# Kernel tuning notes

Hardware: AMD Instinct MI355X
Metric: run time of the kernel (lower is better)

Reference implementation:

```python
import jax, jax.numpy as jnp
import numpy as np
from jax import lax

HEADS, HEAD_DIM, DIM, DIM_OUT, EPS = 12, 64, 768, 768, 1e-5
REL_DIM = 2 * 56 - 1  # 2*max(q_size, kv_size) - 1


def setup_inputs():
    key = jax.random.key(0)
    ks = jax.random.split(key, 10)
    B, T, H, W = 4, 1, 56, 56
    N = 1 + T * H * W
    s = 0.02
    return {
        "x": jax.random.normal(ks[0], (B, N, DIM), jnp.float32),
        "Wqkv": jax.random.normal(ks[1], (DIM, 3 * DIM_OUT), jnp.float32) * s,
        "pool_q_w": jax.random.normal(ks[2], (HEAD_DIM, 1, 3, 3), jnp.float32) * 0.1,
        "pool_k_w": jax.random.normal(ks[3], (HEAD_DIM, 1, 3, 3), jnp.float32) * 0.1,
        "pool_v_w": jax.random.normal(ks[4], (HEAD_DIM, 1, 3, 3), jnp.float32) * 0.1,
        "gq": jnp.ones((HEAD_DIM,), jnp.float32), "bq": jnp.zeros((HEAD_DIM,), jnp.float32),
        "gk": jnp.ones((HEAD_DIM,), jnp.float32), "bk": jnp.zeros((HEAD_DIM,), jnp.float32),
        "gv": jnp.ones((HEAD_DIM,), jnp.float32), "bv": jnp.zeros((HEAD_DIM,), jnp.float32),
        "rel_pos_h": jax.random.normal(ks[5], (REL_DIM, HEAD_DIM), jnp.float32) * s,
        "rel_pos_w": jax.random.normal(ks[6], (REL_DIM, HEAD_DIM), jnp.float32) * s,
        "Wproj": jax.random.normal(ks[7], (DIM_OUT, DIM_OUT), jnp.float32) * s,
        "bproj": jnp.zeros((DIM_OUT,), jnp.float32),
        "T": 1, "H": 56, "W": 56,
    }


def _layernorm(y, g, b):
    mu = y.mean(-1, keepdims=True)
    var = ((y - mu) ** 2).mean(-1, keepdims=True)
    return (y - mu) * lax.rsqrt(var + EPS) * g + b


def _pool(t, w, stride, g, b, B, H, W):
    # t: (B, heads, 1 + H*W, head_dim). Split cls, depthwise conv over spatial body.
    cls, body = t[:, :, :1], t[:, :, 1:]
    y = body.reshape(B * HEADS, H, W, HEAD_DIM).transpose(0, 3, 1, 2)  # (BH, C, H, W)
    y = lax.conv_general_dilated(y, w, (stride, stride), [(1, 1), (1, 1)],
                                 feature_group_count=HEAD_DIM,
                                 dimension_numbers=("NCHW", "OIHW", "NCHW"))
    Ho, Wo = y.shape[2], y.shape[3]
    y = y.reshape(B, HEADS, HEAD_DIM, Ho * Wo).transpose(0, 1, 3, 2)
    y = jnp.concatenate([cls, y], axis=2)
    return _layernorm(y, g, b), Ho, Wo


def _forward(x, Wqkv, pool_q_w, pool_k_w, pool_v_w, gq, bq, gk, bk, gv, bv,
             rel_pos_h, rel_pos_w, Wproj, bproj, T, H, W):
    B, N, _ = x.shape
    scale = HEAD_DIM ** -0.5
    qkv = (x @ Wqkv).reshape(B, N, 3, HEADS, HEAD_DIM).transpose(2, 0, 3, 1, 4)
    q, k, v = qkv[0], qkv[1], qkv[2]  # (B, heads, N, head_dim)
    q, q_h, q_w = _pool(q, pool_q_w, 1, gq, bq, B, H, W)
    k, k_h, k_w = _pool(k, pool_k_w, 2, gk, bk, B, H, W)
    v, _, _ = _pool(v, pool_v_w, 2, gv, bv, B, H, W)
    attn = jnp.einsum("bhqd,bhkd->bhqk", q * scale, k)
    # relative position bias; index tables are static (shapes known at trace time)
    dh = (np.arange(q_h)[:, None] * max(k_h / q_h, 1.0)
          - np.arange(k_h)[None, :] * max(q_h / k_h, 1.0)
          + (k_h - 1) * max(q_h / k_h, 1.0)).astype(np.int32)
    dw = (np.arange(q_w)[:, None] * max(k_w / q_w, 1.0)
          - np.arange(k_w)[None, :] * max(q_w / k_w, 1.0)
          + (k_w - 1) * max(q_w / k_w, 1.0)).astype(np.int32)
    Rh, Rw = rel_pos_h[dh], rel_pos_w[dw]  # (q_h, k_h, c), (q_w, k_w, c)
    r_q = q[:, :, 1:].reshape(B, HEADS, q_h, q_w, HEAD_DIM)
    rel_h = jnp.einsum("byhwc,hkc->byhwk", r_q, Rh)
    rel_w = jnp.einsum("byhwc,wkc->byhwk", r_q, Rw)
    body = (attn[:, :, 1:, 1:].reshape(B, HEADS, q_h, q_w, k_h, k_w)
            + rel_h[..., None] + rel_w[..., None, :])
    attn = attn.at[:, :, 1:, 1:].set(body.reshape(B, HEADS, q_h * q_w, k_h * k_w))
    attn = jax.nn.softmax(attn, axis=-1)
    out = attn @ v
    out = out.at[:, :, 1:, :].add(q[:, :, 1:, :])  # residual pooling (skips cls)
    out = out.transpose(0, 2, 1, 3).reshape(B, -1, DIM_OUT)
    return out @ Wproj + bproj


def reference(x, Wqkv, pool_q_w, pool_k_w, pool_v_w, gq, bq, gk, bk, gv, bv,
              rel_pos_h, rel_pos_w, Wproj, bproj, T, H, W):
    return _forward(x, Wqkv, pool_q_w, pool_k_w, pool_v_w, gq, bq, gk, bk, gv, bv,
                    rel_pos_h, rel_pos_w, Wproj, bproj, T, H, W)
```

## Files before the change

kernel.cpp:

```cpp
#include <hip/hip_runtime.h>
#include <hip/hip_bf16.h>

#define BATCH 4
#define NTOK 3137
#define DIM 768
#define NHEAD 12
#define HD 64
#define QH 56
#define QW 56
#define NKEY 785
#define NKEYPAD 800
#define THREE_DIM 2304
#define MROWS (BATCH*NTOK)
#define QTILE 64
#define NQT 50
#define NBH 48
#define RELROWS (NBH*56)
#define XD 128

#define QSCALE 0.1803368801111204f
#define QUNSCALE 5.5451774444795625f
#define PADSUP  -43.3f

typedef __attribute__((ext_vector_type(8))) short bf16x8;
typedef __attribute__((ext_vector_type(4))) float f32x4;

__device__ __forceinline__ unsigned short f2bf(float f) {
    union { float f; unsigned u; } v; v.f = f;
    unsigned r = v.u + 0x7FFFu + ((v.u >> 16) & 1u);
    return (unsigned short)(r >> 16);
}
__device__ __forceinline__ float bf2f(unsigned short s) {
    union { unsigned u; float f; } v; v.u = (unsigned)s << 16; return v.f;
}
__device__ __forceinline__ int swz64(int x) { return x ^ (((x >> 6) & 7) << 4); }

__device__ __forceinline__ void gl16(const void* g, void* l) {
    __builtin_amdgcn_global_load_lds(
        (const __attribute__((address_space(1))) unsigned int*)g,
        (__attribute__((address_space(3))) unsigned int*)l, 16, 0, 0);
}

__global__ __launch_bounds__(256) void cvt_bf16(
    const float* __restrict__ in, unsigned short* __restrict__ outp, int n4)
{
    for (int i = blockIdx.x * 256 + threadIdx.x; i < n4; i += gridDim.x * 256) {
        float4 v = reinterpret_cast<const float4*>(in)[i];
        union { unsigned short s[4]; uint2 u; } o;
        o.s[0] = f2bf(v.x); o.s[1] = f2bf(v.y);
        o.s[2] = f2bf(v.z); o.s[3] = f2bf(v.w);
        reinterpret_cast<uint2*>(outp)[i] = o.u;
    }
}

__global__ __launch_bounds__(256) void cvt_rel(
    const float* __restrict__ h, const float* __restrict__ w,
    unsigned short* __restrict__ hb, unsigned short* __restrict__ wb)
{
    int i = blockIdx.x * 256 + threadIdx.x;
    const float* src; unsigned short* dst; int j;
    if (i < 1776)      { src = h; dst = hb; j = i; }
    else if (i < 3552) { src = w; dst = wb; j = i - 1776; }
    else return;
    float4 v = reinterpret_cast<const float4*>(src)[j];
    union { unsigned short s[4]; uint2 u; } o;
    o.s[0] = f2bf(v.x); o.s[1] = f2bf(v.y);
    o.s[2] = f2bf(v.z); o.s[3] = f2bf(v.w);
    reinterpret_cast<uint2*>(dst)[j] = o.u;
}

__global__ __launch_bounds__(256) void transpose_bf16_2(
    const float* __restrict__ W0, unsigned short* __restrict__ Wt0,
    const float* __restrict__ W1, unsigned short* __restrict__ Wt1)
{
    const float* W; unsigned short* Wt; int N;
    if (blockIdx.z == 0) { W = W0; Wt = Wt0; N = THREE_DIM; }
    else {
        if (blockIdx.x >= DIM / 32) return;
        W = W1; Wt = Wt1; N = DIM;
    }
    const int K = DIM;
    __shared__ float tile[32][33];
    int k0 = blockIdx.y * 32, n0 = blockIdx.x * 32;
    int t = threadIdx.x;
    int r = t >> 5, c = t & 31;
    #pragma unroll
    for (int p = 0; p < 4; ++p)
        tile[r + p * 8][c] = W[(size_t)(k0 + r + p * 8) * N + n0 + c];
    __syncthreads();
    #pragma unroll
    for (int p = 0; p < 4; ++p)
        Wt[(size_t)(n0 + r + p * 8) * K + k0 + c] = f2bf(tile[c][r + p * 8]);
}

__global__ __launch_bounds__(256, 3) void gemm_mfma(
    const unsigned short* __restrict__ A, const unsigned short* __restrict__ Bt,
    const float* __restrict__ bias, void* __restrict__ C,
    int M, int N, int K, int out_bf16)
{
    __shared__ __align__(16) char lds[49152];
    int t = threadIdx.x;
    int wave = t >> 6, lane = t & 63;
    int lm = lane & 15, lkg = lane >> 4;
    int wr = wave >> 1, wc = wave & 1;

    int gx = gridDim.x;
    int nwg = gx * gridDim.y;
    int lin = blockIdx.y * gx + blockIdx.x;
    int qq = nwg >> 3, rr = nwg & 7;
    int xcd = lin & 7, idx = lin >> 3;
    int newlin = (xcd < rr ? xcd * (qq + 1) : rr * (qq + 1) + (xcd - rr) * qq) + idx;
    int m0 = (newlin / gx) * 128, n0 = (newlin % gx) * 128;

    const unsigned short *gpa0, *gpa1, *gpb0, *gpb1;
    int la0, la1, lb0, lb1;
    {
        int o0 = t * 16, o1 = 4096 + t * 16;
        int r0 = o0 >> 6, s0 = ((o0 >> 4) & 3) ^ ((r0 >> 1) & 3);
        int r1 = o1 >> 6, s1 = ((o1 >> 4) & 3) ^ ((r1 >> 1) & 3);
        int ar0 = m0 + r0; if (ar0 >= M) ar0 = M - 1;
        int ar1 = m0 + r1; if (ar1 >= M) ar1 = M - 1;
        gpa0 = A + (size_t)ar0 * K + s0 * 8;  la0 = o0;
        gpa1 = A + (size_t)ar1 * K + s1 * 8;  la1 = o1;
        gpb0 = Bt + (size_t)(n0 + r0) * K + s0 * 8;  lb0 = 8192 + o0;
        gpb1 = Bt + (size_t)(n0 + r1) * K + s1 * 8;  lb1 = 8192 + o1;
    }

    f32x4 acc[4][4] = {};
    const int nt = K >> 5;

    gl16(gpa0, &lds[la0]); gl16(gpa1, &lds[la1]);
    gl16(gpb0, &lds[lb0]); gl16(gpb1, &lds[lb1]);
    gpa0 += 32; gpa1 += 32; gpb0 += 32; gpb1 += 32;
    gl16(gpa0, &lds[16384 + la0]); gl16(gpa1, &lds[16384 + la1]);
    gl16(gpb0, &lds[16384 + lb0]); gl16(gpb1, &lds[16384 + lb1]);
    gpa0 += 32; gpa1 += 32; gpb0 += 32; gpb1 += 32;

    int cur = 0;
    for (int tt = 0; tt < nt; ++tt) {
        if (tt + 1 < nt) asm volatile("s_waitcnt vmcnt(4)" ::: "memory");
        else             asm volatile("s_waitcnt vmcnt(0)" ::: "memory");
        __builtin_amdgcn_s_barrier();

        if (tt + 2 < nt) {
            int nx = cur + 2; if (nx >= 3) nx -= 3;
            char* nb = &lds[nx << 14];
            gl16(gpa0, nb + la0); gl16(gpa1, nb + la1);
            gl16(gpb0, nb + lb0); gl16(gpb1, nb + lb1);
            gpa0 += 32; gpa1 += 32; gpb0 += 32; gpb1 += 32;
        }

        char* base = &lds[cur << 14];
        bf16x8 af[4], bfr[4];
        #pragma unroll
        for (int m = 0; m < 4; ++m) {
            int row = wr * 64 + m * 16 + lm;
            af[m] = *reinterpret_cast<const bf16x8*>(
                base + row * 64 + ((lkg ^ ((row >> 1) & 3)) << 4));
        }
        #pragma unroll
        for (int n = 0; n < 4; ++n) {
            int row = wc * 64 + n * 16 + lm;
            bfr[n] = *reinterpret_cast<const bf16x8*>(
                base + 8192 + row * 64 + ((lkg ^ ((row >> 1) & 3)) << 4));
        }
        #pragma unroll
        for (int m = 0; m < 4; ++m)
            #pragma unroll
            for (int n = 0; n < 4; ++n)
                acc[m][n] = __builtin_amdgcn_mfma_f32_16x16x32_bf16(
                    af[m], bfr[n], acc[m][n], 0, 0, 0);

        cur = (cur == 2) ? 0 : cur + 1;
    }

    float bv[4];
    #pragma unroll
    for (int n = 0; n < 4; ++n)
        bv[n] = bias ? bias[n0 + wc * 64 + n * 16 + lm] : 0.f;
    #pragma unroll
    for (int m = 0; m < 4; ++m) {
        #pragma unroll
        for (int r = 0; r < 4; ++r) {
            int row = m0 + wr * 64 + m * 16 + lkg * 4 + r;
            if (row >= M) continue;
            #pragma unroll
            for (int n = 0; n < 4; ++n) {
                int col = n0 + wc * 64 + n * 16 + lm;
                float o = acc[m][n][r] + bv[n];
                if (out_bf16)
                    ((unsigned short*)C)[(size_t)row * N + col] = f2bf(o);
                else
                    ((float*)C)[(size_t)row * N + col] = o;
            }
        }
    }
}

__global__ __launch_bounds__(256) void pool_ln_rows(
    const unsigned short* __restrict__ qkvb, const float* __restrict__ w,
    const float* __restrict__ g, const float* __restrict__ beta,
    unsigned short* __restrict__ outp, int qi, int stride, int OH, int OW,
    int mode)
{
    __shared__ unsigned short ibuf[3 * 56 * 64];
    int bid = blockIdx.x;
    int orow = bid % OH;
    int bh = bid / OH;
    int head = bh % NHEAD, b = bh / NHEAD;
    int t = threadIdx.x;
    int wave = t >> 6, lane = t & 63;

    const unsigned short* src =
        qkvb + (size_t)b * NTOK * THREE_DIM + (size_t)qi * DIM + (size_t)head * HD;

    for (int i = t; i < 3 * 56 * 32; i += 256) {
        int pair = i >> 5, off = i & 31;
        int r = pair / 56, iw = pair % 56;
        int ih = orow * stride + r - 1;
        unsigned v = 0;
        if (ih >= 0 && ih < QH)
            v = *reinterpret_cast<const unsigned*>(
                src + (size_t)(1 + ih * QW + iw) * THREE_DIM + off * 2);
        *reinterpret_cast<unsigned*>(&ibuf[pair * 64 + off * 2]) = v;
    }

    float wreg[9];
    #pragma unroll
    for (int k = 0; k < 9; ++k) wreg[k] = w[lane * 9 + k];
    float gl = g[lane], bl = beta[lane];
    __syncthreads();

    int ntask = OW + ((orow == 0) ? 1 : 0);
    for (int task = wave; task < ntask; task += 4) {
        float val;
        int pos;
        if (task == OW) {
            val = bf2f(src[lane]);
            pos = 0;
        } else {
            int ow = task;
            float acc = 0.f;
            #pragma unroll
            for (int r = 0; r < 3; ++r) {
                #pragma unroll
                for (int c = 0; c < 3; ++c) {
                    int iwc = ow * stride + c - 1;
                    if (iwc < 0 || iwc >= QW) continue;
                    acc += bf2f(ibuf[(r * 56 + iwc) * 64 + lane]) * wreg[r * 3 + c];
                }
            }
            val = acc;
            pos = 1 + orow * OW + ow;
        }

        float mu = val;
        #pragma unroll
        for (int off = 32; off > 0; off >>= 1) mu += __shfl_xor(mu, off, 64);
        mu *= (1.f / 64.f);
        float dv = val - mu;
        float var = dv * dv;
        #pragma unroll
        for (int off = 32; off > 0; off >>= 1) var += __shfl_xor(var, off, 64);
        var *= (1.f / 64.f);
        float o = dv * rsqrtf(var + 1e-5f) * gl + bl;

        if (mode == 3) {
            unsigned short* row = outp + ((size_t)bh * NTOK + pos) * XD;
            row[lane] = f2bf(o * QSCALE);
            row[64 + lane] = (lane == 56) ? f2bf(PADSUP) : 0;
        } else if (mode == 1) {
            unsigned short* row = outp + ((size_t)bh * NKEYPAD + pos) * XD;
            row[lane] = f2bf(o);
            unsigned short ext = 0;
            if (pos > 0) {
                int kh = (pos - 1) / 28, kw = (pos - 1) % 28;
                if ((lane < 28 && lane == kh) ||
                    (lane >= 28 && lane < 56 && lane - 28 == kw))
                    ext = 0x3F80;
            }
            row[64 + lane] = ext;
        } else {
            outp[((size_t)bh * HD + lane) * NKEYPAD + pos] = f2bf(o);
        }
    }
}

__global__ __launch_bounds__(64) void pad_kv(
    unsigned short* __restrict__ kpx, unsigned short* __restrict__ vt16)
{
    int bh = blockIdx.x;
    int t = threadIdx.x;
    for (int pos = NKEY; pos < NKEYPAD; ++pos) {
        unsigned short* row = kpx + ((size_t)bh * NKEYPAD + pos) * XD;
        row[t] = 0;
        row[64 + t] = (t == 56) ? 0x3F80 : 0;
        vt16[((size_t)bh * HD + t) * NKEYPAD + pos] = 0;
    }
}

__global__ __launch_bounds__(256) void rel_mfma(
    const unsigned short* __restrict__ qpx, const unsigned short* __restrict__ rh,
    const unsigned short* __restrict__ rw, unsigned short* __restrict__ qpx_out)
{
    __shared__ char bbuf[4096];
    int X = blockIdx.x;
    int m0 = blockIdx.y * 256;
    int mode = blockIdx.z;
    const unsigned short* rtab = mode ? rw : rh;
    int t = threadIdx.x;
    int wave = t >> 6, lane = t & 63;
    int lm = lane & 15, lkg = lane >> 4;

    {
        int row = t >> 3, c8 = t & 7;
        int4 val = {0, 0, 0, 0};
        if (row < 28) {
            int dh = X - 2 * row + 54;
            val = *reinterpret_cast<const int4*>(rtab + (size_t)dh * HD + c8 * 8);
        }
        *reinterpret_cast<int4*>(&bbuf[row * 128 + ((c8 * 16) ^ ((row & 7) << 4))]) = val;
    }
    __syncthreads();

    int rbase = m0 + wave * 64 + lm;
    f32x4 acc[4][2] = {};
    #pragma unroll
    for (int kc = 0; kc < 2; ++kc) {
        bf16x8 bfrag[2];
        #pragma unroll
        for (int nb = 0; nb < 2; ++nb) {
            int row = nb * 16 + lm;
            bfrag[nb] = *reinterpret_cast<const bf16x8*>(
                &bbuf[row * 128 + (((kc * 4 + lkg) * 16) ^ ((row & 7) << 4))]);
        }
        #pragma unroll
        for (int m = 0; m < 4; ++m) {
            int rho = rbase + m * 16; if (rho > RELROWS - 1) rho = RELROWS - 1;
            int bh = rho / 56, rem = rho % 56;
            int pos1 = (mode == 0) ? X * 56 + rem : rem * 56 + X;
            const unsigned short* qsrc =
                qpx + ((size_t)bh * NTOK + 1 + pos1) * XD + kc * 32 + lkg * 8;
            bf16x8 af = *reinterpret_cast<const bf16x8*>(qsrc);
            acc[m][0] = __builtin_amdgcn_mfma_f32_16x16x32_bf16(af, bfrag[0], acc[m][0], 0, 0, 0);
            acc[m][1] = __builtin_amdgcn_mfma_f32_16x16x32_bf16(af, bfrag[1], acc[m][1], 0, 0, 0);
        }
    }

    #pragma unroll
    for (int m = 0; m < 4; ++m) {
        #pragma unroll
        for (int r = 0; r < 4; ++r) {
            int rho = m0 + wave * 64 + m * 16 + lkg * 4 + r;
            if (rho >= RELROWS) continue;
            int bh = rho / 56, rem = rho % 56;
            int pos1 = (mode == 0) ? X * 56 + rem : rem * 56 + X;
            unsigned short* dst =
                qpx_out + ((size_t)bh * NTOK + 1 + pos1) * XD + 64 + mode * 28;
            dst[lm] = f2bf(acc[m][0][r] * 8.f);
            if (lm < 12) dst[16 + lm] = f2bf(acc[m][1][r] * 8.f);
        }
    }
}

__global__ __launch_bounds__(256) void attn_mfma(
    const unsigned short* __restrict__ qpx, const unsigned short* __restrict__ kpx,
    const unsigned short* __restrict__ vt, unsigned short* __restrict__ outp)
{
    __shared__ __align__(16) char kbuf[3][8192];
    __shared__ __align__(16) char vbuf[3][4096];
    __shared__ __align__(16) char pbuf[4][1024];

    int bid0 = blockIdx.x;
    int bid = (bid0 & 7) * ((NBH * NQT) / 8) + (bid0 >> 3);
    int tile = bid % NQT;
    int bh = bid / NQT;
    int head = bh % NHEAD, b = bh / NHEAD;
    int q0 = tile * QTILE;
    int t = threadIdx.x;
    int wave = t >> 6, lane = t & 63;
    int lm = lane & 15, lkg = lane >> 4;

    const unsigned short* kb  = kpx + (size_t)bh * NKEYPAD * XD;
    const unsigned short* vtb = vt + (size_t)bh * HD * NKEYPAD;

    bf16x8 qf[4] = {};
    int qrow = q0 + wave * 16 + lm;
    if (qrow < NTOK) {
        const unsigned short* qs = qpx + ((size_t)bh * NTOK + qrow) * XD + lkg * 8;
        qf[0] = *reinterpret_cast<const bf16x8*>(qs);
        qf[1] = *reinterpret_cast<const bf16x8*>(qs + 32);
        qf[2] = *reinterpret_cast<const bf16x8*>(qs + 64);
        qf[3] = *reinterpret_cast<const bf16x8*>(qs + 96);
    }

    f32x4 oacc[4] = {};
    float osum[4] = {0.f, 0.f, 0.f, 0.f};

    int kr0 = t >> 4;
    int ks0 = (t & 15) ^ (kr0 & 7);
    int kr1 = kr0 + 16;
    const unsigned short* kp0 = kb + (size_t)kr0 * XD + ks0 * 8;
    const unsigned short* kp1 = kb + (size_t)kr1 * XD + ks0 * 8;
    int vr = t >> 2;
    int vs = (t & 3) ^ ((vr >> 1) & 3);
    const unsigned short* vp0 = vtb + (size_t)vr * NKEYPAD + vs * 8;
    int kd0 = wave * 1024, kd1 = 4096 + wave * 1024, vd = wave * 1024;

    const int NT = NKEYPAD / 32;

    gl16(kp0, &kbuf[0][kd0]); gl16(kp1, &kbuf[0][kd1]); gl16(vp0, &vbuf[0][vd]);
    kp0 += 32 * XD; kp1 += 32 * XD; vp0 += 32;
    gl16(kp0, &kbuf[1][kd0]); gl16(kp1, &kbuf[1][kd1]); gl16(vp0, &vbuf[1][vd]);
    kp0 += 32 * XD; kp1 += 32 * XD; vp0 += 32;

    int cur = 0;
    for (int jt = 0; jt < NT; ++jt) {
        if (jt + 1 < NT) asm volatile("s_waitcnt vmcnt(3)" ::: "memory");
        else             asm volatile("s_waitcnt vmcnt(0)" ::: "memory");
        __builtin_amdgcn_s_barrier();

        f32x4 acc0 = {0.f, 0.f, 0.f, 0.f}, acc1 = {0.f, 0.f, 0.f, 0.f};
        #pragma unroll
        for (int kc = 0; kc < 4; ++kc) {
            int sl = (kc * 4 + lkg) ^ (lm & 7);
            bf16x8 kf0 = *reinterpret_cast<const bf16x8*>(&kbuf[cur][lm * 256 + sl * 16]);
            acc0 = __builtin_amdgcn_mfma_f32_16x16x32_bf16(qf[kc], kf0, acc0, 0, 0, 0);
            bf16x8 kf1 = *reinterpret_cast<const bf16x8*>(&kbuf[cur][(16 + lm) * 256 + sl * 16]);
            acc1 = __builtin_amdgcn_mfma_f32_16x16x32_bf16(qf[kc], kf1, acc1, 0, 0, 0);
        }

        if (jt + 2 < NT) {
            int nx = cur + 2; if (nx >= 3) nx -= 3;
            gl16(kp0, &kbuf[nx][kd0]);
            gl16(kp1, &kbuf[nx][kd1]);
            gl16(vp0, &vbuf[nx][vd]);
            kp0 += 32 * XD; kp1 += 32 * XD; vp0 += 32;
        }

        #pragma unroll
        for (int nb = 0; nb < 2; ++nb) {
            f32x4 a = nb ? acc1 : acc0;
            #pragma unroll
            for (int r = 0; r < 4; ++r) {
                float e;
                asm("v_exp_f32 %0, %1" : "=v"(e) : "v"(a[r]));
                osum[r] += e;
                union { float f; unsigned u; } ue; ue.f = e;
                int baddr = (lkg * 4 + r) * 64 + (nb * 16 + lm) * 2;
                *reinterpret_cast<unsigned short*>(&pbuf[wave][swz64(baddr)]) =
                    (unsigned short)(ue.u >> 16);
            }
        }

        bf16x8 pf = *reinterpret_cast<const bf16x8*>(&pbuf[wave][swz64(lm * 64 + lkg * 16)]);
        #pragma unroll
        for (int db = 0; db < 4; ++db) {
            int row = db * 16 + lm;
            bf16x8 vf = *reinterpret_cast<const bf16x8*>(
                &vbuf[cur][row * 64 + ((lkg ^ ((row >> 1) & 3)) << 4)]);
            oacc[db] = __builtin_amdgcn_mfma_f32_16x16x32_bf16(pf, vf, oacc[db], 0, 0, 0);
        }

        cur = (cur == 2) ? 0 : cur + 1;
    }

    #pragma unroll
    for (int r = 0; r < 4; ++r) {
        float s = osum[r];
        s += __shfl_xor(s, 1, 64);
        s += __shfl_xor(s, 2, 64);
        s += __shfl_xor(s, 4, 64);
        s += __shfl_xor(s, 8, 64);
        osum[r] = 1.f / s;
    }
    #pragma unroll
    for (int r = 0; r < 4; ++r) {
        int qpos = q0 + wave * 16 + lkg * 4 + r;
        if (qpos >= NTOK) continue;
        unsigned short* orow = outp + ((size_t)b * NTOK + qpos) * DIM + (size_t)head * HD;
        const unsigned short* qres = qpx + ((size_t)bh * NTOK + qpos) * XD;
        #pragma unroll
        for (int db = 0; db < 4; ++db) {
            int d = db * 16 + lm;
            float o = oacc[db][r] * osum[r];
            if (qpos > 0) o += bf2f(qres[d]) * QUNSCALE;
            orow[d] = f2bf(o);
        }
    }
}

extern "C" void kernel_launch(void* const* d_in, const int* in_sizes, int n_in,
                              void* d_out, int out_size, void* d_ws, size_t ws_size,
                              hipStream_t stream) {
    const float* x     = (const float*)d_in[0];
    const float* Wqkv  = (const float*)d_in[1];
    const float* pqw   = (const float*)d_in[2];
    const float* pkw   = (const float*)d_in[3];
    const float* pvw   = (const float*)d_in[4];
    const float* gq    = (const float*)d_in[5];
    const float* bq    = (const float*)d_in[6];
    const float* gk    = (const float*)d_in[7];
    const float* bk    = (const float*)d_in[8];
    const float* gv    = (const float*)d_in[9];
    const float* bv    = (const float*)d_in[10];
    const float* rph   = (const float*)d_in[11];
    const float* rpw   = (const float*)d_in[12];
    const float* Wproj = (const float*)d_in[13];
    const float* bproj = (const float*)d_in[14];

    unsigned short* qkvb  = (unsigned short*)d_ws;
    unsigned short* qpx   = qkvb + (size_t)MROWS * THREE_DIM;
    unsigned short* kpx   = qpx + (size_t)NBH * NTOK * XD;
    unsigned short* vt16  = kpx + (size_t)NBH * NKEYPAD * XD;
    unsigned short* xbf   = vt16 + (size_t)NBH * HD * NKEYPAD;
    unsigned short* wqkvt = xbf + (size_t)MROWS * DIM;
    unsigned short* wprojt= wqkvt + (size_t)DIM * THREE_DIM;
    unsigned short* rphb  = wprojt + (size_t)DIM * DIM;
    unsigned short* rpwb  = rphb + 7104;
    unsigned short* attn_bf = qkvb;

    dim3 blk(256);

    cvt_bf16<<<2048, blk, 0, stream>>>(x, xbf, (int)((size_t)MROWS * DIM / 4));
    {
        dim3 g(THREE_DIM / 32, DIM / 32, 2);
        transpose_bf16_2<<<g, blk, 0, stream>>>(Wqkv, wqkvt, Wproj, wprojt);
    }
    cvt_rel<<<14, blk, 0, stream>>>(rph, rpw, rphb, rpwb);

    {
        dim3 grid(THREE_DIM / 128, (MROWS + 127) / 128);
        gemm_mfma<<<grid, blk, 0, stream>>>(xbf, wqkvt, nullptr, qkvb,
                                            MROWS, THREE_DIM, DIM, 1);
    }

    pool_ln_rows<<<NBH * QH, blk, 0, stream>>>(qkvb, pqw, gq, bq, qpx,  0, 1, QH, QW, 3);
    pool_ln_rows<<<NBH * 28, blk, 0, stream>>>(qkvb, pkw, gk, bk, kpx,  1, 2, 28, 28, 1);
    pool_ln_rows<<<NBH * 28, blk, 0, stream>>>(qkvb, pvw, gv, bv, vt16, 2, 2, 28, 28, 2);
    pad_kv<<<NBH, 64, 0, stream>>>(kpx, vt16);

    {
        dim3 g(56, (RELROWS + 255) / 256, 2);
        rel_mfma<<<g, blk, 0, stream>>>(qpx, rphb, rpwb, qpx);
    }

    attn_mfma<<<NBH * NQT, blk, 0, stream>>>(qpx, kpx, vt16, attn_bf);

    {
        dim3 grid(DIM / 128, (MROWS + 127) / 128);
        gemm_mfma<<<grid, blk, 0, stream>>>(attn_bf, wprojt, bproj, d_out,
                                            MROWS, DIM, DIM, 0);
    }
}
```

Before: 295.2 us.

## Double attention query tile to 128 with 8 waves, merge K/V pooling launches

```diff
diff --git a/kernel.cpp b/kernel.cpp
--- a/kernel.cpp
+++ b/kernel.cpp
@@ -12,8 +12,8 @@
 #define NKEYPAD 800
 #define THREE_DIM 2304
 #define MROWS (BATCH*NTOK)
-#define QTILE 64
-#define NQT 50
+#define QT2 128
+#define NQT2 25
 #define NBH 48
 #define RELROWS (NBH*56)
 #define XD 128
@@ -33,7 +33,6 @@
 __device__ __forceinline__ float bf2f(unsigned short s) {
     union { unsigned u; float f; } v; v.u = (unsigned)s << 16; return v.f;
 }
-__device__ __forceinline__ int swz64(int x) { return x ^ (((x >> 6) & 7) << 4); }
 
 __device__ __forceinline__ void gl16(const void* g, void* l) {
     __builtin_amdgcn_global_load_lds(
@@ -164,12 +163,14 @@
             bfr[n] = *reinterpret_cast<const bf16x8*>(
                 base + 8192 + row * 64 + ((lkg ^ ((row >> 1) & 3)) << 4));
         }
+        __builtin_amdgcn_s_setprio(1);
         #pragma unroll
         for (int m = 0; m < 4; ++m)
             #pragma unroll
             for (int n = 0; n < 4; ++n)
                 acc[m][n] = __builtin_amdgcn_mfma_f32_16x16x32_bf16(
                     af[m], bfr[n], acc[m][n], 0, 0, 0);
+        __builtin_amdgcn_s_setprio(0);
 
         cur = (cur == 2) ? 0 : cur + 1;
     }
@@ -197,23 +198,12 @@
     }
 }
 
-__global__ __launch_bounds__(256) void pool_ln_rows(
-    const unsigned short* __restrict__ qkvb, const float* __restrict__ w,
-    const float* __restrict__ g, const float* __restrict__ beta,
-    unsigned short* __restrict__ outp, int qi, int stride, int OH, int OW,
-    int mode)
-{
-    __shared__ unsigned short ibuf[3 * 56 * 64];
-    int bid = blockIdx.x;
-    int orow = bid % OH;
-    int bh = bid / OH;
-    int head = bh % NHEAD, b = bh / NHEAD;
-    int t = threadIdx.x;
-    int wave = t >> 6, lane = t & 63;
-
-    const unsigned short* src =
-        qkvb + (size_t)b * NTOK * THREE_DIM + (size_t)qi * DIM + (size_t)head * HD;
-
+__device__ __forceinline__ void pool_body(
+    const unsigned short* src, const float* w, const float* g,
+    const float* beta, unsigned short* outp, int bh, int orow,
+    int stride, int OW, int mode, unsigned short* ibuf,
+    int t, int wave, int lane)
+{
     for (int i = t; i < 3 * 56 * 32; i += 256) {
         int pair = i >> 5, off = i & 31;
         int r = pair / 56, iw = pair % 56;
@@ -286,6 +276,45 @@
     }
 }
 
+__global__ __launch_bounds__(256) void pool_ln_q(
+    const unsigned short* __restrict__ qkvb, const float* __restrict__ w,
+    const float* __restrict__ g, const float* __restrict__ beta,
+    unsigned short* __restrict__ outp)
+{
+    __shared__ unsigned short ibuf[3 * 56 * 64];
+    int bid = blockIdx.x;
+    int orow = bid % QH;
+    int bh = bid / QH;
+    int head = bh % NHEAD, b = bh / NHEAD;
+    const unsigned short* src =
+        qkvb + (size_t)b * NTOK * THREE_DIM + (size_t)head * HD;
+    pool_body(src, w, g, beta, outp, bh, orow, 1, QW, 3, ibuf,
+              threadIdx.x, threadIdx.x >> 6, threadIdx.x & 63);
+}
+
+__global__ __launch_bounds__(256) void pool_ln_kv(
+    const unsigned short* __restrict__ qkvb,
+    const float* __restrict__ wk, const float* __restrict__ gk,
+    const float* __restrict__ bk, unsigned short* __restrict__ kpx,
+    const float* __restrict__ wv, const float* __restrict__ gv,
+    const float* __restrict__ bv, unsigned short* __restrict__ vt16)
+{
+    __shared__ unsigned short ibuf[3 * 56 * 64];
+    int bid = blockIdx.x;
+    int orow = bid % 28;
+    int bh = bid / 28;
+    int head = bh % NHEAD, b = bh / NHEAD;
+    int isv = blockIdx.y;
+    const unsigned short* src = qkvb + (size_t)b * NTOK * THREE_DIM
+        + (size_t)(isv ? 2 : 1) * DIM + (size_t)head * HD;
+    if (isv)
+        pool_body(src, wv, gv, bv, vt16, bh, orow, 2, 28, 2, ibuf,
+                  threadIdx.x, threadIdx.x >> 6, threadIdx.x & 63);
+    else
+        pool_body(src, wk, gk, bk, kpx, bh, orow, 2, 28, 1, ibuf,
+                  threadIdx.x, threadIdx.x >> 6, threadIdx.x & 63);
+}
+
 __global__ __launch_bounds__(64) void pad_kv(
     unsigned short* __restrict__ kpx, unsigned short* __restrict__ vt16)
 {
@@ -363,20 +392,20 @@
     }
 }
 
-__global__ __launch_bounds__(256) void attn_mfma(
+__global__ __launch_bounds__(512, 4) void attn_mfma(
     const unsigned short* __restrict__ qpx, const unsigned short* __restrict__ kpx,
     const unsigned short* __restrict__ vt, unsigned short* __restrict__ outp)
 {
     __shared__ __align__(16) char kbuf[3][8192];
     __shared__ __align__(16) char vbuf[3][4096];
-    __shared__ __align__(16) char pbuf[4][1024];
+    __shared__ __align__(16) char pbuf[8][1024];
 
     int bid0 = blockIdx.x;
-    int bid = (bid0 & 7) * ((NBH * NQT) / 8) + (bid0 >> 3);
-    int tile = bid % NQT;
-    int bh = bid / NQT;
+    int bid = (bid0 & 7) * ((NBH * NQT2) / 8) + (bid0 >> 3);
+    int tile = bid % NQT2;
+    int bh = bid / NQT2;
     int head = bh % NHEAD, b = bh / NHEAD;
-    int q0 = tile * QTILE;
+    int q0 = tile * QT2;
     int t = threadIdx.x;
     int wave = t >> 6, lane = t & 63;
     int lm = lane & 15, lkg = lane >> 4;
@@ -397,30 +426,41 @@
     f32x4 oacc[4] = {};
     float osum[4] = {0.f, 0.f, 0.f, 0.f};
 
-    int kr0 = t >> 4;
-    int ks0 = (t & 15) ^ (kr0 & 7);
-    int kr1 = kr0 + 16;
-    const unsigned short* kp0 = kb + (size_t)kr0 * XD + ks0 * 8;
-    const unsigned short* kp1 = kb + (size_t)kr1 * XD + ks0 * 8;
-    int vr = t >> 2;
-    int vs = (t & 3) ^ ((vr >> 1) & 3);
+    int kr = t >> 4;
+    int ks = (t & 15) ^ (kr & 7);
+    const unsigned short* kp0 = kb + (size_t)kr * XD + ks * 8;
+    int kd = t * 16;
+    int vidx = t & 255;
+    int vr = vidx >> 2;
+    int vs = (vidx & 3) ^ ((vr >> 1) & 3);
     const unsigned short* vp0 = vtb + (size_t)vr * NKEYPAD + vs * 8;
-    int kd0 = wave * 1024, kd1 = 4096 + wave * 1024, vd = wave * 1024;
+    int vd = vidx * 16;
 
     const int NT = NKEYPAD / 32;
 
-    gl16(kp0, &kbuf[0][kd0]); gl16(kp1, &kbuf[0][kd1]); gl16(vp0, &vbuf[0][vd]);
-    kp0 += 32 * XD; kp1 += 32 * XD; vp0 += 32;
-    gl16(kp0, &kbuf[1][kd0]); gl16(kp1, &kbuf[1][kd1]); gl16(vp0, &vbuf[1][vd]);
-    kp0 += 32 * XD; kp1 += 32 * XD; vp0 += 32;
+    int pwa = (lkg << 5) + ((lm >> 3) << 4) + (lm & 7) * 2;
+    int pra = ((lm >> 2) << 5) + ((lkg & 1) << 4) + ((lm & 3) << 7) + ((lkg >> 1) << 9);
+
+    gl16(kp0, &kbuf[0][kd]); gl16(vp0, &vbuf[0][vd]);
+    kp0 += 32 * XD; vp0 += 32;
+    gl16(kp0, &kbuf[1][kd]); gl16(vp0, &vbuf[1][vd]);
+    kp0 += 32 * XD; vp0 += 32;
 
     int cur = 0;
     for (int jt = 0; jt < NT; ++jt) {
-        if (jt + 1 < NT) asm volatile("s_waitcnt vmcnt(3)" ::: "memory");
+        if (jt + 1 < NT) asm volatile("s_waitcnt vmcnt(2)" ::: "memory");
         else             asm volatile("s_waitcnt vmcnt(0)" ::: "memory");
         __builtin_amdgcn_s_barrier();
 
+        if (jt + 2 < NT) {
+            int nx = cur + 2; if (nx >= 3) nx -= 3;
+            gl16(kp0, &kbuf[nx][kd]);
+            gl16(vp0, &vbuf[nx][vd]);
+            kp0 += 32 * XD; vp0 += 32;
+        }
+
         f32x4 acc0 = {0.f, 0.f, 0.f, 0.f}, acc1 = {0.f, 0.f, 0.f, 0.f};
+        __builtin_amdgcn_s_setprio(1);
         #pragma unroll
         for (int kc = 0; kc < 4; ++kc) {
             int sl = (kc * 4 + lkg) ^ (lm & 7);
@@ -429,14 +469,7 @@
             bf16x8 kf1 = *reinterpret_cast<const bf16x8*>(&kbuf[cur][(16 + lm) * 256 + sl * 16]);
             acc1 = __builtin_amdgcn_mfma_f32_16x16x32_bf16(qf[kc], kf1, acc1, 0, 0, 0);
         }
-
-        if (jt + 2 < NT) {
-            int nx = cur + 2; if (nx >= 3) nx -= 3;
-            gl16(kp0, &kbuf[nx][kd0]);
-            gl16(kp1, &kbuf[nx][kd1]);
-            gl16(vp0, &vbuf[nx][vd]);
-            kp0 += 32 * XD; kp1 += 32 * XD; vp0 += 32;
-        }
+        __builtin_amdgcn_s_setprio(0);
 
         #pragma unroll
         for (int nb = 0; nb < 2; ++nb) {
@@ -447,13 +480,14 @@
                 asm("v_exp_f32 %0, %1" : "=v"(e) : "v"(a[r]));
                 osum[r] += e;
                 union { float f; unsigned u; } ue; ue.f = e;
-                int baddr = (lkg * 4 + r) * 64 + (nb * 16 + lm) * 2;
-                *reinterpret_cast<unsigned short*>(&pbuf[wave][swz64(baddr)]) =
+                *reinterpret_cast<unsigned short*>(
+                    &pbuf[wave][pwa + (r << 7) + (nb << 9)]) =
                     (unsigned short)(ue.u >> 16);
             }
         }
 
-        bf16x8 pf = *reinterpret_cast<const bf16x8*>(&pbuf[wave][swz64(lm * 64 + lkg * 16)]);
+        bf16x8 pf = *reinterpret_cast<const bf16x8*>(&pbuf[wave][pra]);
+        __builtin_amdgcn_s_setprio(1);
         #pragma unroll
         for (int db = 0; db < 4; ++db) {
             int row = db * 16 + lm;
@@ -461,6 +495,7 @@
                 &vbuf[cur][row * 64 + ((lkg ^ ((row >> 1) & 3)) << 4)]);
             oacc[db] = __builtin_amdgcn_mfma_f32_16x16x32_bf16(pf, vf, oacc[db], 0, 0, 0);
         }
+        __builtin_amdgcn_s_setprio(0);
 
         cur = (cur == 2) ? 0 : cur + 1;
     }
@@ -535,9 +570,12 @@
                                             MROWS, THREE_DIM, DIM, 1);
     }
 
-    pool_ln_rows<<<NBH * QH, blk, 0, stream>>>(qkvb, pqw, gq, bq, qpx,  0, 1, QH, QW, 3);
-    pool_ln_rows<<<NBH * 28, blk, 0, stream>>>(qkvb, pkw, gk, bk, kpx,  1, 2, 28, 28, 1);
-    pool_ln_rows<<<NBH * 28, blk, 0, stream>>>(qkvb, pvw, gv, bv, vt16, 2, 2, 28, 28, 2);
+    pool_ln_q<<<NBH * QH, blk, 0, stream>>>(qkvb, pqw, gq, bq, qpx);
+    {
+        dim3 g(NBH * 28, 2);
+        pool_ln_kv<<<g, blk, 0, stream>>>(qkvb, pkw, gk, bk, kpx,
+                                          pvw, gv, bv, vt16);
+    }
     pad_kv<<<NBH, 64, 0, stream>>>(kpx, vt16);
 
     {
@@ -545,7 +583,7 @@
         rel_mfma<<<g, blk, 0, stream>>>(qpx, rphb, rpwb, qpx);
     }
 
-    attn_mfma<<<NBH * NQT, blk, 0, stream>>>(qpx, kpx, vt16, attn_bf);
+    attn_mfma<<<NBH * NQT2, 512, 0, stream>>>(qpx, kpx, vt16, attn_bf);
 
     {
         dim3 grid(DIM / 128, (MROWS + 127) / 128);
```

After: 278.0 us. 1.06x faster.
